# Kernel optimization log

Measured on AMD Instinct MI355X. Metric: run time of the kernel, lower is better.

Reference implementation:

```python
import jax, jax.numpy as jnp
import numpy as np

N = 30000      # nodes
E = 1000000    # edges
G = 256        # graphs
IN = 3         # in_channels
H = 8          # heads
D = 16         # per-head dim
HID = 128      # hidden_dim = H*D
L = 3          # num_layers
KP = 17        # num_keypoints
KPE = 16       # kp_emb_dim
NEG = 0.2      # GATv2 leaky_relu negative slope
EPS = 1e-5     # BatchNorm eps


def setup_inputs() -> dict:
    key = jax.random.key(0)
    ks = jax.random.split(key, 24)
    x = jax.random.normal(ks[0], (N, IN), jnp.float32)
    edge_index = jax.random.randint(ks[1], (2, E), 0, N, jnp.int32)
    batch = jnp.sort(jax.random.randint(ks[2], (N,), 0, G, jnp.int32))
    s_in = 1.0 / np.sqrt(IN + KPE)
    s_h = 1.0 / np.sqrt(HID)
    return {
        "x": x,
        "edge_index": edge_index,
        "batch": batch,
        "kp_emb": jax.random.normal(ks[3], (KP, KPE), jnp.float32),
        "w_in": jax.random.normal(ks[4], (IN + KPE, HID), jnp.float32) * s_in,
        "b_in": jax.random.normal(ks[5], (HID,), jnp.float32) * 0.01,
        "w_l": jax.random.normal(ks[6], (L, HID, HID), jnp.float32) * s_h,
        "w_r": jax.random.normal(ks[7], (L, HID, HID), jnp.float32) * s_h,
        "att": jax.random.normal(ks[8], (L, H, D), jnp.float32) * (1.0 / np.sqrt(D)),
        "conv_bias": jax.random.normal(ks[9], (L, HID), jnp.float32) * 0.01,
        "bn_gamma": jnp.ones((L, HID), jnp.float32) + 0.1 * jax.random.normal(ks[10], (L, HID), jnp.float32),
        "bn_beta": 0.1 * jax.random.normal(ks[11], (L, HID), jnp.float32),
        "bn_mean": 0.1 * jax.random.normal(ks[12], (L, HID), jnp.float32),
        "bn_var": 0.5 + jax.random.uniform(ks[13], (L, HID), jnp.float32),
        "w1": jax.random.normal(ks[14], (HID, 2 * HID), jnp.float32) * s_h,
        "b1": jnp.zeros((2 * HID,), jnp.float32),
        "w2": jax.random.normal(ks[15], (2 * HID, HID), jnp.float32) * (1.0 / np.sqrt(2 * HID)),
        "b2": jnp.zeros((HID,), jnp.float32),
        "w3": jax.random.normal(ks[16], (HID, 2), jnp.float32) * s_h,
        "b3": jnp.zeros((2,), jnp.float32),
    }


def reference(x, edge_index, batch, kp_emb, w_in, b_in, w_l, w_r, att, conv_bias,
              bn_gamma, bn_beta, bn_mean, bn_var, w1, b1, w2, b2, w3, b3):
    n = x.shape[0]
    # keypoint id embedding concat + input projection
    kp_ids = jnp.arange(n) % KP
    h = jnp.concatenate([x, kp_emb[kp_ids]], axis=-1) @ w_in + b_in  # [N, HID]
    # GATv2Conv adds self loops by default
    loops = jnp.arange(n, dtype=edge_index.dtype)
    src = jnp.concatenate([edge_index[0], loops])  # message sources (j)
    dst = jnp.concatenate([edge_index[1], loops])  # message targets (i)
    for l in range(L):
        xl = (h @ w_l[l]).reshape(n, H, D)  # source transform (lin_l)
        xr = (h @ w_r[l]).reshape(n, H, D)  # target transform (lin_r)
        z = xl[src] + xr[dst]                              # [Et, H, D]
        score = jnp.einsum('ehd,hd->eh', jax.nn.leaky_relu(z, NEG), att[l])
        # segment softmax over incoming edges of each dst node
        m = jax.ops.segment_max(score, dst, num_segments=n)
        ex = jnp.exp(score - m[dst])
        denom = jax.ops.segment_sum(ex, dst, num_segments=n)
        alpha = ex / denom[dst]                            # [Et, H]
        msg = xl[src] * alpha[..., None]                   # [Et, H, D]
        out = jax.ops.segment_sum(msg, dst, num_segments=n).reshape(n, HID) + conv_bias[l]
        out = jax.nn.relu(out)
        # BatchNorm1d (eval mode: running stats)
        out = (out - bn_mean[l]) * (bn_gamma[l] / jnp.sqrt(bn_var[l] + EPS)) + bn_beta[l]
        h = h + out  # residual (dropout = identity in eval)
    # global mean pool per graph
    sums = jax.ops.segment_sum(h, batch, num_segments=G)
    cnt = jax.ops.segment_sum(jnp.ones((n, 1), h.dtype), batch, num_segments=G)
    g = sums / jnp.maximum(cnt, 1.0)
    # classifier MLP
    g = jax.nn.elu(g @ w1 + b1)
    g = jax.nn.elu(g @ w2 + b2)
    return g @ w3 + b3  # [G, 2]
```

## Files before the change

### kernel.cpp

```cpp
#include <hip/hip_runtime.h>
#include <hip/hip_bf16.h>

#define N_NODES 30000
#define N_EDGES 1000000
#define N_GRAPHS 256
#define HEADS 8
#define DHEAD 16
#define HIDDEN 128
#define LAYERS 3
#define KPN 17
#define KPE 16
#define NEG_SLOPE 0.2f
#define BN_EPS 1e-5f
#define ET (N_EDGES + N_NODES)
#define NBIN 235
#define BINW 128
#define BINCAP 6016
#define CHUNK 4096
#define NB_EDGE 245
#define NBG 1876

typedef __attribute__((ext_vector_type(8))) short bf16x8;
typedef __attribute__((ext_vector_type(4))) float f32x4;

__device__ __forceinline__ unsigned bf16_rne(float f) {
    unsigned u = __float_as_uint(f);
    return (u + 0x7fffu + ((u >> 16) & 1u)) >> 16;
}
__device__ __forceinline__ float bf16_lo(unsigned w) { return __uint_as_float(w << 16); }
__device__ __forceinline__ float bf16_hi(unsigned w) { return __uint_as_float(w & 0xffff0000u); }

__global__ __launch_bounds__(256) void k_pre(const int* __restrict__ batch,
                                             int* __restrict__ bcnt,
                                             int* __restrict__ gptr,
                                             int* __restrict__ ptr,
                                             const float* __restrict__ w_l,
                                             const float* __restrict__ w_r,
                                             const float* __restrict__ kp_emb,
                                             const float* __restrict__ w_in,
                                             const float* __restrict__ b_in,
                                             unsigned short* __restrict__ wT,
                                             float* __restrict__ kpp) {
    int bid = blockIdx.x, t = threadIdx.x;
    if (bid == 0) {
        if (t < NBIN) bcnt[t] = 0;
        for (int g = t; g <= N_GRAPHS; g += 256) {
            if (g == N_GRAPHS) { gptr[g] = N_NODES; }
            else {
                int lo = 0, hi = N_NODES;
                while (lo < hi) {
                    int mid = (lo + hi) >> 1;
                    if (batch[mid] < g) lo = mid + 1; else hi = mid;
                }
                gptr[g] = lo;
            }
        }
        if (t == 0) ptr[N_NODES] = ET;
    } else if (bid <= 384) {
        int idx = (bid - 1) * 256 + t;
        if (idx < LAYERS * 256 * 128) {
            int l = idx / (256 * 128);
            int rem = idx - l * 256 * 128;
            int c = rem >> 7;
            int k = rem & 127;
            float v = (c < 128) ? w_l[(size_t)l * 16384 + k * 128 + c]
                                : w_r[(size_t)l * 16384 + k * 128 + (c - 128)];
            wT[idx] = (unsigned short)bf16_rne(v);
        }
    } else {
        int idx = (bid - 385) * 256 + t;
        if (idx < KPN * 128) {
            int p = idx >> 7, c = idx & 127;
            float acc = b_in[c];
#pragma unroll
            for (int k = 0; k < KPE; ++k)
                acc += kp_emb[p * KPE + k] * w_in[(3 + k) * 128 + c];
            kpp[idx] = acc;
        }
    }
}

template<bool FUSED>
__global__ __launch_bounds__(256) void k_gemmT(const float* __restrict__ x,
                                               const float* __restrict__ kpp,
                                               const float* __restrict__ w_in,
                                               unsigned short* __restrict__ hb_out,
                                               const unsigned short* __restrict__ hb,
                                               const unsigned short* __restrict__ wT,
                                               unsigned short* __restrict__ xlb,
                                               unsigned short* __restrict__ xrb,
                                               const int* __restrict__ ei,
                                               int* __restrict__ bcnt,
                                               unsigned* __restrict__ bdata) {
    __shared__ unsigned short st[32][132];
    __shared__ unsigned short hsA[FUSED ? 32 : 1][136];
    __shared__ int lcnt[FUSED ? NBIN : 1];
    __shared__ int lbase[FUSED ? NBIN : 1];
    int tid = threadIdx.x;

    if (FUSED && blockIdx.x < NB_EDGE) {
        int base = blockIdx.x * CHUNK;
        int n = N_EDGES - base; if (n > CHUNK) n = CHUNK;
        for (int i = tid; i < NBIN; i += 256) lcnt[i] = 0;
        __syncthreads();
        for (int t = tid; t < n; t += 256) {
            int d = ei[N_EDGES + base + t];
            atomicAdd(&lcnt[d >> 7], 1);
        }
        __syncthreads();
        for (int i = tid; i < NBIN; i += 256) {
            int c = lcnt[i];
            lbase[i] = c ? atomicAdd(&bcnt[i], c) : 0;
            lcnt[i] = 0;
        }
        __syncthreads();
        for (int t = tid; t < n; t += 256) {
            int s = ei[base + t];
            int d = ei[N_EDGES + base + t];
            int b = d >> 7;
            int pos = lbase[b] + atomicAdd(&lcnt[b], 1);
            bdata[(size_t)b * BINCAP + pos] = (unsigned)s | ((unsigned)(d & 127) << 15);
        }
        return;
    }

    int gbid = FUSED ? (blockIdx.x - NB_EDGE) : blockIdx.x;
    int half = gbid & 1;
    int brow = (gbid >> 1) * 32;
    int wave = tid >> 6, lane = tid & 63;
    int lr = lane & 15, lk = lane >> 4;

    if (FUSED) {
        int r = tid >> 3, c16 = (tid & 7) * 16;
        int gr = brow + r;
        int gc = gr < N_NODES ? gr : 0;
        float xv0 = x[gc * 3], xv1 = x[gc * 3 + 1], xv2 = x[gc * 3 + 2];
        const float* kprow = kpp + (gc % KPN) * 128;
        float res[16];
#pragma unroll
        for (int q = 0; q < 16; ++q) {
            int c = c16 + q;
            res[q] = kprow[c] + xv0 * w_in[c] + xv1 * w_in[128 + c] + xv2 * w_in[256 + c];
        }
        unsigned short pk16[16];
#pragma unroll
        for (int q = 0; q < 16; ++q) pk16[q] = (unsigned short)bf16_rne(res[q]);
        if (gr < N_NODES && half == 0) {
            *(uint4*)(hb_out + (size_t)gr * 128 + c16)     = *(uint4*)&pk16[0];
            *(uint4*)(hb_out + (size_t)gr * 128 + c16 + 8) = *(uint4*)&pk16[8];
        }
#pragma unroll
        for (int q = 0; q < 16; ++q) hsA[r][c16 + q] = pk16[q];
        __syncthreads();
    }

    int ar0c = brow + lr;      if (ar0c >= N_NODES) ar0c = N_NODES - 1;
    int ar1c = brow + 16 + lr; if (ar1c >= N_NODES) ar1c = N_NODES - 1;
    int c0l = wave * 32 + lr;
    const unsigned short* wb = wT + (size_t)(half * 128 + c0l) * 128 + lk * 8;

    f32x4 acc[2][2];
#pragma unroll
    for (int m = 0; m < 2; ++m)
#pragma unroll
        for (int n = 0; n < 2; ++n) acc[m][n] = (f32x4){0.f, 0.f, 0.f, 0.f};

#pragma unroll
    for (int ks = 0; ks < 4; ++ks) {
        bf16x8 a0, a1;
        if (FUSED) {
            a0 = *(const bf16x8*)&hsA[lr][lk * 8 + ks * 32];
            a1 = *(const bf16x8*)&hsA[16 + lr][lk * 8 + ks * 32];
        } else {
            a0 = *(const bf16x8*)(hb + (size_t)ar0c * 128 + lk * 8 + ks * 32);
            a1 = *(const bf16x8*)(hb + (size_t)ar1c * 128 + lk * 8 + ks * 32);
        }
#pragma unroll
        for (int nt = 0; nt < 2; ++nt) {
            bf16x8 b = *(const bf16x8*)(wb + nt * 16 * 128 + ks * 32);
            acc[0][nt] = __builtin_amdgcn_mfma_f32_16x16x32_bf16(a0, b, acc[0][nt], 0, 0, 0);
            acc[1][nt] = __builtin_amdgcn_mfma_f32_16x16x32_bf16(a1, b, acc[1][nt], 0, 0, 0);
        }
    }

    int r0 = lk * 4;
#pragma unroll
    for (int mt = 0; mt < 2; ++mt)
#pragma unroll
        for (int nt = 0; nt < 2; ++nt)
#pragma unroll
            for (int j = 0; j < 4; ++j)
                st[mt * 16 + r0 + j][c0l + nt * 16] = (unsigned short)bf16_rne(acc[mt][nt][j]);
    __syncthreads();

    int rr = tid >> 3, seg = tid & 7;
    int grow = brow + rr;
    if (grow < N_NODES) {
        unsigned short* dst = (half == 0 ? xlb : xrb) + (size_t)grow * 128 + seg * 16;
        *(uint4*)(dst)     = *(uint4*)&st[rr][seg * 16];
        *(uint4*)(dst + 8) = *(uint4*)&st[rr][seg * 16 + 8];
    }
}

__global__ __launch_bounds__(256) void k_place2(const int* __restrict__ bcnt,
                                                const unsigned* __restrict__ bdata,
                                                int* __restrict__ ptr,
                                                unsigned short* __restrict__ csr_src) {
    __shared__ int vsc[256];
    __shared__ unsigned ldata[BINCAP];
    __shared__ unsigned short lcsr[BINCAP + BINW];
    __shared__ int hist[BINW], pre[BINW], nodestart[BINW], lofs[BINW];
    __shared__ int bbase_sh;
    int b = blockIdx.x, tid = threadIdx.x;
    int n = bcnt[b];
    int nNodes = N_NODES - b * BINW; if (nNodes > BINW) nNodes = BINW;

    for (int t = tid; t < n; t += 256) ldata[t] = bdata[(size_t)b * BINCAP + t];

    int c = 0;
    if (tid < NBIN) {
        int nodes = N_NODES - tid * BINW; if (nodes > BINW) nodes = BINW;
        c = bcnt[tid] + nodes;
    }
    vsc[tid] = c;
    if (tid < BINW) hist[tid] = (tid < nNodes) ? 1 : 0;
    __syncthreads();
    for (int off = 1; off < 256; off <<= 1) {
        int x = (tid >= off) ? vsc[tid - off] : 0;
        __syncthreads();
        vsc[tid] += x;
        __syncthreads();
    }
    if (tid == 0) bbase_sh = (b == 0) ? 0 : vsc[b - 1];

    for (int t = tid; t < n; t += 256)
        atomicAdd(&hist[(ldata[t] >> 15) & 127], 1);
    __syncthreads();
    if (tid < BINW) pre[tid] = hist[tid];
    __syncthreads();
    for (int off = 1; off < BINW; off <<= 1) {
        int x = (tid >= off && tid < BINW) ? pre[tid - off] : 0;
        __syncthreads();
        if (tid < BINW) pre[tid] += x;
        __syncthreads();
    }
    if (tid < BINW) {
        int ns = pre[tid] - hist[tid];
        nodestart[tid] = ns;
        if (tid < nNodes) {
            int node = b * BINW + tid;
            ptr[node] = bbase_sh + ns;
            lcsr[ns] = (unsigned short)node;
        }
        lofs[tid] = 1;
    }
    __syncthreads();
    for (int t = tid; t < n; t += 256) {
        unsigned e = ldata[t];
        int dl = (e >> 15) & 127;
        int pos = nodestart[dl] + atomicAdd(&lofs[dl], 1);
        lcsr[pos] = (unsigned short)(e & 0x7fffu);
    }
    __syncthreads();
    int tot = n + nNodes;
    for (int t = tid; t < tot; t += 256) csr_src[bbase_sh + t] = lcsr[t];
}

__global__ __launch_bounds__(256) void k_gat(const unsigned* __restrict__ xlb,
                                             const unsigned* __restrict__ xrb,
                                             const int* __restrict__ ptr,
                                             const unsigned short* __restrict__ csr_src,
                                             const float* __restrict__ att_l,
                                             const float* __restrict__ bias_l,
                                             const float* __restrict__ gamma_l,
                                             const float* __restrict__ beta_l,
                                             const float* __restrict__ mean_l,
                                             const float* __restrict__ var_l,
                                             unsigned* __restrict__ hb32) {
    int wid = (blockIdx.x * 256 + threadIdx.x) >> 6;
    int lane = threadIdx.x & 63;
    if (wid >= N_NODES) return;
    int i = wid;
    int grp = lane >> 5;
    int l32 = lane & 31;
    int d0 = 4 * l32;

    uint2 xw = *(const uint2*)(xrb + ((size_t)i << 6) + (l32 << 1));
    float xr0 = bf16_lo(xw.x), xr1 = bf16_hi(xw.x);
    float xr2 = bf16_lo(xw.y), xr3 = bf16_hi(xw.y);
    const float L2E = 1.44269504089f;
    float4 av = *(const float4*)(att_l + d0);
    av.x *= L2E; av.y *= L2E; av.z *= L2E; av.w *= L2E;
    int e0 = ptr[i], e1 = ptr[i + 1];

    float denom = 0.f, acc0 = 0.f, acc1 = 0.f, acc2 = 0.f, acc3 = 0.f;

#define LDP(KP, WREG, VREG) { \
    int eo = 2 * (KP) + grp; \
    int sr = __shfl(sv, eo); \
    VREG = eo < cnt; \
    int rw = VREG ? sr : 0; \
    WREG = *(const uint2*)(xlb + ((size_t)rw << 6) + (l32 << 1)); \
}
#define PROCP(WREG, VREG) { \
    float v0 = bf16_lo(WREG.x), v1 = bf16_hi(WREG.x); \
    float v2 = bf16_lo(WREG.y), v3 = bf16_hi(WREG.y); \
    float z0 = v0 + xr0, z1 = v1 + xr1, z2 = v2 + xr2, z3 = v3 + xr3; \
    z0 = fmaxf(z0, NEG_SLOPE * z0); \
    z1 = fmaxf(z1, NEG_SLOPE * z1); \
    z2 = fmaxf(z2, NEG_SLOPE * z2); \
    z3 = fmaxf(z3, NEG_SLOPE * z3); \
    float p = z0 * av.x + z1 * av.y + z2 * av.z + z3 * av.w; \
    p += __shfl_xor(p, 1); \
    p += __shfl_xor(p, 2); \
    float ex = VREG ? exp2f(p) : 0.f; \
    denom += ex; \
    acc0 += ex * v0; acc1 += ex * v1; acc2 += ex * v2; acc3 += ex * v3; \
}

    for (int base = e0; base < e1; base += 64) {
        int idx = base + lane;
        int sv = (idx < e1) ? (int)csr_src[idx] : 0;
        int cnt = e1 - base; if (cnt > 64) cnt = 64;
        int np = (cnt + 1) >> 1;

        uint2 w0, w1; bool b0 = false, b1 = false;
        LDP(0, w0, b0);
        if (1 < np) LDP(1, w1, b1);
        int k = 0;
        for (; k + 2 < np; k += 2) {
            uint2 n0, n1; bool c0v, c1v;
            LDP(k + 2, n0, c0v);
            LDP(k + 3, n1, c1v);
            PROCP(w0, b0); PROCP(w1, b1);
            w0 = n0; b0 = c0v; w1 = n1; b1 = c1v;
        }
        PROCP(w0, b0);
        if (k + 1 < np) PROCP(w1, b1);
    }
#undef LDP
#undef PROCP

    denom += __shfl_xor(denom, 32);
    acc0 += __shfl_xor(acc0, 32);
    acc1 += __shfl_xor(acc1, 32);
    acc2 += __shfl_xor(acc2, 32);
    acc3 += __shfl_xor(acc3, 32);

    if (grp == 0) {
        float inv = 1.f / denom;
        float4 bia = *(const float4*)(bias_l + d0);
        float4 gam = *(const float4*)(gamma_l + d0);
        float4 bet = *(const float4*)(beta_l + d0);
        float4 mea = *(const float4*)(mean_l + d0);
        float4 var = *(const float4*)(var_l + d0);
        float o0 = fmaxf(acc0 * inv + bia.x, 0.f);
        float o1 = fmaxf(acc1 * inv + bia.y, 0.f);
        float o2 = fmaxf(acc2 * inv + bia.z, 0.f);
        float o3 = fmaxf(acc3 * inv + bia.w, 0.f);
        o0 = (o0 - mea.x) * (gam.x * rsqrtf(var.x + BN_EPS)) + bet.x;
        o1 = (o1 - mea.y) * (gam.y * rsqrtf(var.y + BN_EPS)) + bet.y;
        o2 = (o2 - mea.z) * (gam.z * rsqrtf(var.z + BN_EPS)) + bet.z;
        o3 = (o3 - mea.w) * (gam.w * rsqrtf(var.w + BN_EPS)) + bet.w;
        unsigned* hp = hb32 + ((size_t)i << 6) + (l32 << 1);
        uint2 hw = *(const uint2*)hp;
        float h0 = bf16_lo(hw.x), h1 = bf16_hi(hw.x);
        float h2 = bf16_lo(hw.y), h3 = bf16_hi(hw.y);
        h0 += o0; h1 += o1; h2 += o2; h3 += o3;
        uint2 pk;
        pk.x = bf16_rne(h0) | (bf16_rne(h1) << 16);
        pk.y = bf16_rne(h2) | (bf16_rne(h3) << 16);
        *(uint2*)hp = pk;
    }
}

__global__ __launch_bounds__(256) void k_poolmlp(const unsigned short* __restrict__ hb,
                                                 const int* __restrict__ gptr,
                                                 const float* __restrict__ w1, const float* __restrict__ b1,
                                                 const float* __restrict__ w2, const float* __restrict__ b2,
                                                 const float* __restrict__ w3, const float* __restrict__ b3,
                                                 float* __restrict__ out) {
    __shared__ float red[256];
    __shared__ float g[128], t1[256], t2[128];
    int b = blockIdx.x, t = threadIdx.x;
    int c = t & 127, half = t >> 7;
    int lo = gptr[b], hi = gptr[b + 1];
    float s = 0.f;
    for (int i = lo + half; i < hi; i += 2)
        s += __uint_as_float((unsigned)hb[(size_t)i * 128 + c] << 16);
    red[t] = s;
    __syncthreads();
    if (half == 0) {
        float cntf = fmaxf((float)(hi - lo), 1.0f);
        g[c] = (red[c] + red[c + 128]) / cntf;
    }
    __syncthreads();
    {
        float acc = b1[t];
        for (int k = 0; k < 128; ++k) acc += g[k] * w1[k * 256 + t];
        t1[t] = acc > 0.f ? acc : expm1f(acc);
    }
    __syncthreads();
    if (t < 128) {
        float acc = b2[t];
        for (int k = 0; k < 256; ++k) acc += t1[k] * w2[k * 128 + t];
        t2[t] = acc > 0.f ? acc : expm1f(acc);
    }
    __syncthreads();
    if (t < 2) {
        float acc = b3[t];
        for (int k = 0; k < 128; ++k) acc += t2[k] * w3[k * 2 + t];
        out[b * 2 + t] = acc;
    }
}

extern "C" void kernel_launch(void* const* d_in, const int* in_sizes, int n_in,
                              void* d_out, int out_size, void* d_ws, size_t ws_size,
                              hipStream_t stream) {
    const float* x        = (const float*)d_in[0];
    const int*   ei       = (const int*)d_in[1];
    const int*   batch    = (const int*)d_in[2];
    const float* kp_emb   = (const float*)d_in[3];
    const float* w_in     = (const float*)d_in[4];
    const float* b_in     = (const float*)d_in[5];
    const float* w_l      = (const float*)d_in[6];
    const float* w_r      = (const float*)d_in[7];
    const float* att      = (const float*)d_in[8];
    const float* conv_b   = (const float*)d_in[9];
    const float* bn_gamma = (const float*)d_in[10];
    const float* bn_beta  = (const float*)d_in[11];
    const float* bn_mean  = (const float*)d_in[12];
    const float* bn_var   = (const float*)d_in[13];
    const float* w1 = (const float*)d_in[14];
    const float* b1 = (const float*)d_in[15];
    const float* w2 = (const float*)d_in[16];
    const float* b2 = (const float*)d_in[17];
    const float* w3 = (const float*)d_in[18];
    const float* b3 = (const float*)d_in[19];
    float* out = (float*)d_out;

    char* ws = (char*)d_ws;
    const size_t OFF_HB   = 0;
    const size_t OFF_XL   = OFF_HB   + 7680000;
    const size_t OFF_XR   = OFF_XL   + 7680000;
    const size_t OFF_WT   = OFF_XR   + 7680000;
    const size_t OFF_PTR  = OFF_WT   + 196608;
    const size_t OFF_BCNT = OFF_PTR  + 120320;
    const size_t OFF_SRC  = OFF_BCNT + 1024;
    const size_t OFF_GPTR = OFF_SRC  + 2060032;
    const size_t OFF_BD   = OFF_GPTR + 1088;
    const size_t OFF_KPP  = OFF_BD   + (size_t)NBIN * BINCAP * 4;

    unsigned short* hb     = (unsigned short*)(ws + OFF_HB);
    unsigned short* xlb    = (unsigned short*)(ws + OFF_XL);
    unsigned short* xrb    = (unsigned short*)(ws + OFF_XR);
    unsigned short* wT     = (unsigned short*)(ws + OFF_WT);
    int*            ptr    = (int*)(ws + OFF_PTR);
    int*            bcnt   = (int*)(ws + OFF_BCNT);
    unsigned short* csrsrc = (unsigned short*)(ws + OFF_SRC);
    int*            gptr   = (int*)(ws + OFF_GPTR);
    unsigned*       bdata  = (unsigned*)(ws + OFF_BD);
    float*          kpp    = (float*)(ws + OFF_KPP);

    k_pre<<<385 + (KPN * 128 + 255) / 256, 256, 0, stream>>>(
        batch, bcnt, gptr, ptr, w_l, w_r, kp_emb, w_in, b_in, wT, kpp);

    k_gemmT<true><<<NB_EDGE + NBG, 256, 0, stream>>>(
        x, kpp, w_in, hb, hb, wT, xlb, xrb, ei, bcnt, bdata);

    k_place2<<<NBIN, 256, 0, stream>>>(bcnt, bdata, ptr, csrsrc);

    for (int l = 0; l < LAYERS; ++l) {
        if (l > 0) {
            k_gemmT<false><<<NBG, 256, 0, stream>>>(
                x, kpp, w_in, hb, hb, wT + (size_t)l * 256 * 128, xlb, xrb,
                ei, bcnt, bdata);
        }
        k_gat<<<(N_NODES + 3) / 4, 256, 0, stream>>>(
            (const unsigned*)xlb, (const unsigned*)xrb, ptr, csrsrc,
            att + (size_t)l * 128, conv_b + (size_t)l * 128,
            bn_gamma + (size_t)l * 128, bn_beta + (size_t)l * 128,
            bn_mean + (size_t)l * 128, bn_var + (size_t)l * 128,
            (unsigned*)hb);
    }

    k_poolmlp<<<N_GRAPHS, 256, 0, stream>>>(hb, gptr, w1, b1, w2, b2, w3, b3, out);
}
```

Before: 236.0 us.

## Shift edge binning into k_pre and fuse CSR placement into the first GEMM launch

Edge binning by destination moves from the first fused GEMM kernel into the preprocessing kernel. The CSR placement kernel is folded into the first GEMM launch as extra blocks, which saves a kernel launch and lets placement run alongside the input-projection GEMM. The bin counter reset becomes a hipMemsetAsync, which adds a small API call. Placement now reads bdata from global memory twice instead of staging it in shared memory, and the non-fused GEMM now stages its A rows in shared memory before the MFMA loop.

Result: no change. 235.8 us (-0.1%).

```diff
diff --git a/kernel.cpp b/kernel.cpp
--- a/kernel.cpp
+++ b/kernel.cpp
@@ -19,6 +19,9 @@
 #define CHUNK 4096
 #define NB_EDGE 245
 #define NBG 1876
+#define PRE_MISC 1
+#define PRE_WCONV 384
+#define PRE_KPP 9
 
 typedef __attribute__((ext_vector_type(8))) short bf16x8;
 typedef __attribute__((ext_vector_type(4))) float f32x4;
@@ -40,10 +43,13 @@
                                              const float* __restrict__ w_in,
                                              const float* __restrict__ b_in,
                                              unsigned short* __restrict__ wT,
-                                             float* __restrict__ kpp) {
+                                             float* __restrict__ kpp,
+                                             const int* __restrict__ ei,
+                                             unsigned* __restrict__ bdata) {
+    __shared__ int lcnt[NBIN];
+    __shared__ int lbase[NBIN];
     int bid = blockIdx.x, t = threadIdx.x;
     if (bid == 0) {
-        if (t < NBIN) bcnt[t] = 0;
         for (int g = t; g <= N_GRAPHS; g += 256) {
             if (g == N_GRAPHS) { gptr[g] = N_NODES; }
             else {
@@ -56,7 +62,7 @@
             }
         }
         if (t == 0) ptr[N_NODES] = ET;
-    } else if (bid <= 384) {
+    } else if (bid <= PRE_WCONV) {
         int idx = (bid - 1) * 256 + t;
         if (idx < LAYERS * 256 * 128) {
             int l = idx / (256 * 128);
@@ -67,8 +73,8 @@
                                 : w_r[(size_t)l * 16384 + k * 128 + (c - 128)];
             wT[idx] = (unsigned short)bf16_rne(v);
         }
-    } else {
-        int idx = (bid - 385) * 256 + t;
+    } else if (bid <= PRE_WCONV + PRE_KPP) {
+        int idx = (bid - PRE_WCONV - 1) * 256 + t;
         if (idx < KPN * 128) {
             int p = idx >> 7, c = idx & 127;
             float acc = b_in[c];
@@ -76,6 +82,29 @@
             for (int k = 0; k < KPE; ++k)
                 acc += kp_emb[p * KPE + k] * w_in[(3 + k) * 128 + c];
             kpp[idx] = acc;
+        }
+    } else {
+        int base = (bid - PRE_WCONV - PRE_KPP - 1) * CHUNK;
+        int n = N_EDGES - base; if (n > CHUNK) n = CHUNK;
+        for (int i = t; i < NBIN; i += 256) lcnt[i] = 0;
+        __syncthreads();
+        for (int q = t; q < n; q += 256) {
+            int d = ei[N_EDGES + base + q];
+            atomicAdd(&lcnt[d >> 7], 1);
+        }
+        __syncthreads();
+        for (int i = t; i < NBIN; i += 256) {
+            int c = lcnt[i];
+            lbase[i] = c ? atomicAdd(&bcnt[i], c) : 0;
+            lcnt[i] = 0;
+        }
+        __syncthreads();
+        for (int q = t; q < n; q += 256) {
+            int s = ei[base + q];
+            int d = ei[N_EDGES + base + q];
+            int b = d >> 7;
+            int pos = lbase[b] + atomicAdd(&lcnt[b], 1);
+            bdata[(size_t)b * BINCAP + pos] = (unsigned)s | ((unsigned)(d & 127) << 15);
         }
     }
 }
@@ -89,42 +118,80 @@
                                                const unsigned short* __restrict__ wT,
                                                unsigned short* __restrict__ xlb,
                                                unsigned short* __restrict__ xrb,
-                                               const int* __restrict__ ei,
-                                               int* __restrict__ bcnt,
-                                               unsigned* __restrict__ bdata) {
-    __shared__ unsigned short st[32][132];
-    __shared__ unsigned short hsA[FUSED ? 32 : 1][136];
-    __shared__ int lcnt[FUSED ? NBIN : 1];
-    __shared__ int lbase[FUSED ? NBIN : 1];
+                                               const int* __restrict__ bcnt,
+                                               const unsigned* __restrict__ bdata,
+                                               int* __restrict__ ptr,
+                                               unsigned short* __restrict__ csr_src) {
+    __shared__ char smem[17408];
+    unsigned short (*st)[136]  = (unsigned short(*)[136])smem;
+    unsigned short (*hsA)[136] = (unsigned short(*)[136])(smem + 8704);
     int tid = threadIdx.x;
 
-    if (FUSED && blockIdx.x < NB_EDGE) {
-        int base = blockIdx.x * CHUNK;
-        int n = N_EDGES - base; if (n > CHUNK) n = CHUNK;
-        for (int i = tid; i < NBIN; i += 256) lcnt[i] = 0;
-        __syncthreads();
-        for (int t = tid; t < n; t += 256) {
-            int d = ei[N_EDGES + base + t];
-            atomicAdd(&lcnt[d >> 7], 1);
-        }
-        __syncthreads();
-        for (int i = tid; i < NBIN; i += 256) {
-            int c = lcnt[i];
-            lbase[i] = c ? atomicAdd(&bcnt[i], c) : 0;
-            lcnt[i] = 0;
-        }
-        __syncthreads();
-        for (int t = tid; t < n; t += 256) {
-            int s = ei[base + t];
-            int d = ei[N_EDGES + base + t];
-            int b = d >> 7;
-            int pos = lbase[b] + atomicAdd(&lcnt[b], 1);
-            bdata[(size_t)b * BINCAP + pos] = (unsigned)s | ((unsigned)(d & 127) << 15);
-        }
+    if (FUSED && blockIdx.x < NBIN) {
+        int* vsc        = (int*)smem;
+        int* hist       = (int*)(smem + 1024);
+        int* pre        = (int*)(smem + 1536);
+        int* nodestart  = (int*)(smem + 2048);
+        int* lofs       = (int*)(smem + 2560);
+        int* bbase_sh   = (int*)(smem + 3072);
+        unsigned short* lcsr = (unsigned short*)(smem + 3088);
+
+        int b = blockIdx.x;
+        int n = bcnt[b];
+        int nNodes = N_NODES - b * BINW; if (nNodes > BINW) nNodes = BINW;
+
+        int c = 0;
+        if (tid < NBIN) {
+            int nodes = N_NODES - tid * BINW; if (nodes > BINW) nodes = BINW;
+            c = bcnt[tid] + nodes;
+        }
+        vsc[tid] = c;
+        if (tid < BINW) hist[tid] = (tid < nNodes) ? 1 : 0;
+        __syncthreads();
+        for (int off = 1; off < 256; off <<= 1) {
+            int xv = (tid >= off) ? vsc[tid - off] : 0;
+            __syncthreads();
+            vsc[tid] += xv;
+            __syncthreads();
+        }
+        if (tid == 0) *bbase_sh = (b == 0) ? 0 : vsc[b - 1];
+
+        for (int q = tid; q < n; q += 256)
+            atomicAdd(&hist[(bdata[(size_t)b * BINCAP + q] >> 15) & 127], 1);
+        __syncthreads();
+        if (tid < BINW) pre[tid] = hist[tid];
+        __syncthreads();
+        for (int off = 1; off < BINW; off <<= 1) {
+            int xv = (tid >= off && tid < BINW) ? pre[tid - off] : 0;
+            __syncthreads();
+            if (tid < BINW) pre[tid] += xv;
+            __syncthreads();
+        }
+        if (tid < BINW) {
+            int ns = pre[tid] - hist[tid];
+            nodestart[tid] = ns;
+            if (tid < nNodes) {
+                int node = b * BINW + tid;
+                ptr[node] = *bbase_sh + ns;
+                lcsr[ns] = (unsigned short)node;
+            }
+            lofs[tid] = 1;
+        }
+        __syncthreads();
+        for (int q = tid; q < n; q += 256) {
+            unsigned e = bdata[(size_t)b * BINCAP + q];
+            int dl = (e >> 15) & 127;
+            int pos = nodestart[dl] + atomicAdd(&lofs[dl], 1);
+            lcsr[pos] = (unsigned short)(e & 0x7fffu);
+        }
+        __syncthreads();
+        int tot = n + nNodes;
+        int bb = *bbase_sh;
+        for (int q = tid; q < tot; q += 256) csr_src[bb + q] = lcsr[q];
         return;
     }
 
-    int gbid = FUSED ? (blockIdx.x - NB_EDGE) : blockIdx.x;
+    int gbid = FUSED ? (blockIdx.x - NBIN) : blockIdx.x;
     int half = gbid & 1;
     int brow = (gbid >> 1) * 32;
     int wave = tid >> 6, lane = tid & 63;
@@ -151,11 +218,15 @@
         }
 #pragma unroll
         for (int q = 0; q < 16; ++q) hsA[r][c16 + q] = pk16[q];
-        __syncthreads();
-    }
-
-    int ar0c = brow + lr;      if (ar0c >= N_NODES) ar0c = N_NODES - 1;
-    int ar1c = brow + 16 + lr; if (ar1c >= N_NODES) ar1c = N_NODES - 1;
+    } else {
+        int r = tid >> 3, seg = tid & 7;
+        int gr = brow + r; if (gr >= N_NODES) gr = N_NODES - 1;
+        const unsigned short* srcp = hb + (size_t)gr * 128 + seg * 16;
+        *(uint4*)&hsA[r][seg * 16]     = *(const uint4*)srcp;
+        *(uint4*)&hsA[r][seg * 16 + 8] = *(const uint4*)(srcp + 8);
+    }
+    __syncthreads();
+
     int c0l = wave * 32 + lr;
     const unsigned short* wb = wT + (size_t)(half * 128 + c0l) * 128 + lk * 8;
 
@@ -167,14 +238,8 @@
 
 #pragma unroll
     for (int ks = 0; ks < 4; ++ks) {
-        bf16x8 a0, a1;
-        if (FUSED) {
-            a0 = *(const bf16x8*)&hsA[lr][lk * 8 + ks * 32];
-            a1 = *(const bf16x8*)&hsA[16 + lr][lk * 8 + ks * 32];
-        } else {
-            a0 = *(const bf16x8*)(hb + (size_t)ar0c * 128 + lk * 8 + ks * 32);
-            a1 = *(const bf16x8*)(hb + (size_t)ar1c * 128 + lk * 8 + ks * 32);
-        }
+        bf16x8 a0 = *(const bf16x8*)&hsA[lr][lk * 8 + ks * 32];
+        bf16x8 a1 = *(const bf16x8*)&hsA[16 + lr][lk * 8 + ks * 32];
 #pragma unroll
         for (int nt = 0; nt < 2; ++nt) {
             bf16x8 b = *(const bf16x8*)(wb + nt * 16 * 128 + ks * 32);
@@ -200,70 +265,6 @@
         *(uint4*)(dst)     = *(uint4*)&st[rr][seg * 16];
         *(uint4*)(dst + 8) = *(uint4*)&st[rr][seg * 16 + 8];
     }
-}
-
-__global__ __launch_bounds__(256) void k_place2(const int* __restrict__ bcnt,
-                                                const unsigned* __restrict__ bdata,
-                                                int* __restrict__ ptr,
-                                                unsigned short* __restrict__ csr_src) {
-    __shared__ int vsc[256];
-    __shared__ unsigned ldata[BINCAP];
-    __shared__ unsigned short lcsr[BINCAP + BINW];
-    __shared__ int hist[BINW], pre[BINW], nodestart[BINW], lofs[BINW];
-    __shared__ int bbase_sh;
-    int b = blockIdx.x, tid = threadIdx.x;
-    int n = bcnt[b];
-    int nNodes = N_NODES - b * BINW; if (nNodes > BINW) nNodes = BINW;
-
-    for (int t = tid; t < n; t += 256) ldata[t] = bdata[(size_t)b * BINCAP + t];
-
-    int c = 0;
-    if (tid < NBIN) {
-        int nodes = N_NODES - tid * BINW; if (nodes > BINW) nodes = BINW;
-        c = bcnt[tid] + nodes;
-    }
-    vsc[tid] = c;
-    if (tid < BINW) hist[tid] = (tid < nNodes) ? 1 : 0;
-    __syncthreads();
-    for (int off = 1; off < 256; off <<= 1) {
-        int x = (tid >= off) ? vsc[tid - off] : 0;
-        __syncthreads();
-        vsc[tid] += x;
-        __syncthreads();
-    }
-    if (tid == 0) bbase_sh = (b == 0) ? 0 : vsc[b - 1];
-
-    for (int t = tid; t < n; t += 256)
-        atomicAdd(&hist[(ldata[t] >> 15) & 127], 1);
-    __syncthreads();
-    if (tid < BINW) pre[tid] = hist[tid];
-    __syncthreads();
-    for (int off = 1; off < BINW; off <<= 1) {
-        int x = (tid >= off && tid < BINW) ? pre[tid - off] : 0;
-        __syncthreads();
-        if (tid < BINW) pre[tid] += x;
-        __syncthreads();
-    }
-    if (tid < BINW) {
-        int ns = pre[tid] - hist[tid];
-        nodestart[tid] = ns;
-        if (tid < nNodes) {
-            int node = b * BINW + tid;
-            ptr[node] = bbase_sh + ns;
-            lcsr[ns] = (unsigned short)node;
-        }
-        lofs[tid] = 1;
-    }
-    __syncthreads();
-    for (int t = tid; t < n; t += 256) {
-        unsigned e = ldata[t];
-        int dl = (e >> 15) & 127;
-        int pos = nodestart[dl] + atomicAdd(&lofs[dl], 1);
-        lcsr[pos] = (unsigned short)(e & 0x7fffu);
-    }
-    __syncthreads();
-    int tot = n + nNodes;
-    for (int t = tid; t < tot; t += 256) csr_src[bbase_sh + t] = lcsr[t];
 }
 
 __global__ __launch_bounds__(256) void k_gat(const unsigned* __restrict__ xlb,
@@ -462,19 +463,19 @@
     unsigned*       bdata  = (unsigned*)(ws + OFF_BD);
     float*          kpp    = (float*)(ws + OFF_KPP);
 
-    k_pre<<<385 + (KPN * 128 + 255) / 256, 256, 0, stream>>>(
-        batch, bcnt, gptr, ptr, w_l, w_r, kp_emb, w_in, b_in, wT, kpp);
-
-    k_gemmT<true><<<NB_EDGE + NBG, 256, 0, stream>>>(
-        x, kpp, w_in, hb, hb, wT, xlb, xrb, ei, bcnt, bdata);
-
-    k_place2<<<NBIN, 256, 0, stream>>>(bcnt, bdata, ptr, csrsrc);
+    hipMemsetAsync(bcnt, 0, NBIN * 4, stream);
+
+    k_pre<<<PRE_MISC + PRE_WCONV + PRE_KPP + NB_EDGE, 256, 0, stream>>>(
+        batch, bcnt, gptr, ptr, w_l, w_r, kp_emb, w_in, b_in, wT, kpp, ei, bdata);
+
+    k_gemmT<true><<<NBIN + NBG, 256, 0, stream>>>(
+        x, kpp, w_in, hb, hb, wT, xlb, xrb, bcnt, bdata, ptr, csrsrc);
 
     for (int l = 0; l < LAYERS; ++l) {
         if (l > 0) {
             k_gemmT<false><<<NBG, 256, 0, stream>>>(
                 x, kpp, w_in, hb, hb, wT + (size_t)l * 256 * 128, xlb, xrb,
-                ei, bcnt, bdata);
+                bcnt, bdata, ptr, csrsrc);
         }
         k_gat<<<(N_NODES + 3) / 4, 256, 0, stream>>>(
             (const unsigned*)xlb, (const unsigned*)xrb, ptr, csrsrc,
```
